# Performance work log

Measured on AMD Instinct MI355X. Metric: run time of the kernel, lower is better.

## Reference

```python
import jax, jax.numpy as jnp
import numpy as np

# init_kwargs constants
ALPHA = 0.1
BETA = 0.1
CAPACITY = 1000.0
IDX_LNN = 0   # feat_idx['ln(N+1)']
IDX_DOBS = 2  # feat_idx['D_observed']
IDX_RATE = 3  # feat_idx['pkt_rate']

N = 4_194_304
W = 4096  # number of windows (static upper bound on window ids)
EPS = 1e-6


def _masked_quantile75(vals, valid):
    """torch.quantile(vals[valid], 0.75) with linear interpolation, jit-safe."""
    s = jnp.sort(jnp.where(valid, vals, jnp.inf))
    n = jnp.sum(valid)
    pos = jnp.maximum(0.75 * (n - 1).astype(jnp.float32), 0.0)
    lo = jnp.floor(pos).astype(jnp.int32)
    hi = jnp.ceil(pos).astype(jnp.int32)
    frac = pos - lo.astype(jnp.float32)
    q = s[lo] * (1.0 - frac) + s[hi] * frac
    return jnp.where(n > 0, jnp.maximum(q, EPS), 1.0)


def setup_inputs() -> dict:
    key = jax.random.key(0)
    k1, k2, k3, k4, k5 = jax.random.split(key, 5)
    logits = jax.random.normal(k1, (N, 2), jnp.float32)
    y = jax.random.randint(k2, (N,), 0, 2)
    mask = jnp.ones((N,), bool)
    x_raw = jax.random.normal(k3, (N, 4), jnp.float32)
    window_idx = jax.random.randint(k4, (N,), 0, W)
    class_weights = jax.random.uniform(k5, (2,), jnp.float32, 0.5, 1.5)
    return {"logits": logits, "y": y, "mask": mask, "x_raw": x_raw,
            "window_idx": window_idx, "class_weights": class_weights}


def reference(logits, y, mask, x_raw, window_idx, class_weights):
    maskf = mask.astype(jnp.float32)
    any_mask = jnp.sum(maskf) > 0

    # L_data: weighted cross entropy over masked samples
    logp = jax.nn.log_softmax(logits, axis=1)
    nll = -jnp.take_along_axis(logp, y[:, None], axis=1)[:, 0]
    wy = class_weights[y]
    denom = jnp.sum(maskf * wy)
    l_data = jnp.sum(maskf * wy * nll) / jnp.maximum(denom, 1e-12)

    # per-window physics terms (vectorized segment reductions)
    valid = (window_idx >= 0) & mask
    vf = valid.astype(jnp.float32)
    attack_prob = jax.nn.softmax(logits, axis=1)[:, 1]
    flow_rate = jnp.maximum(x_raw[:, IDX_RATE], 0.0)
    d_obs = jnp.maximum(x_raw[:, IDX_DOBS], 0.0)
    # note: flow_vol (exp(lnN)-1) is computed in the original but never used in the loss

    ref_dobs = _masked_quantile75(d_obs, valid)

    seg = jnp.where(valid, window_idx, 0).astype(jnp.int32)
    pv = attack_prob * vf  # zeroed contributions for invalid rows
    cnt = jax.ops.segment_sum(vf, seg, num_segments=W)
    sum_p = jax.ops.segment_sum(pv, seg, num_segments=W)
    agg_rate = jax.ops.segment_sum(pv * flow_rate, seg, num_segments=W)
    sum_pd = jax.ops.segment_sum(pv * d_obs, seg, num_segments=W)

    include = ((cnt >= 2.0) & (sum_p >= EPS)).astype(jnp.float32)

    d_mean = sum_pd / (sum_p + EPS)
    rate_ratio = agg_rate / (CAPACITY + EPS)
    buildup = jax.nn.relu(rate_ratio - 1.0)
    flow_t = buildup * buildup
    rho = jnp.clip(rate_ratio, 0.0, 0.99)
    d_theory = 1.0 / (1.0 - rho + EPS)
    lat_t = jax.nn.relu(d_theory - d_mean / ref_dobs)

    n_inc = jnp.sum(include)
    safe_n = jnp.maximum(n_inc, 1.0)
    l_flow = jnp.where(n_inc > 0, jnp.sum(flow_t * include) / safe_n, 0.0)
    l_latency = jnp.where(n_inc > 0, jnp.sum(lat_t * include) / safe_n, 0.0)

    # empty-mask early return path
    l_data = jnp.where(any_mask, l_data, 0.0)
    l_flow = jnp.where(any_mask, l_flow, 0.0)
    l_latency = jnp.where(any_mask, l_latency, 0.0)
    l_total = l_data + ALPHA * l_flow + BETA * l_latency
    return (l_total, l_data, l_flow, l_latency)
```

## Files before the change

### kernel.cpp

```cpp
#include <hip/hip_runtime.h>

#define NWIN 4096
#define EPSF 1e-6f
#define GRID_MAIN 512
#define BLOCK_MAIN 512
#define NWAVES (BLOCK_MAIN / 64)

#define SCALE_P   2097152.0f
#define SCALE_R   131072.0f
#define INV_P     (1.0/2097152.0)
#define INV_R     (1.0/131072.0)

#define OFF_SEGU  256
#define OFF_H1    65792
#define OFF_H2    73984
#define OFF_H3    90368
#define OFF_CEP   98560
#define OFF_PART  131072

__device__ __forceinline__ unsigned make_key_raw(const float2* __restrict__ xzw,
                                                 const int* __restrict__ mask,
                                                 const int* __restrict__ widx, int i)
{
    int wi = widx[i];
    int m = mask[i];
    if (wi < 0 || !m) return 0x7F800000u;
    float d = fmaxf(xzw[2 * i + 1].x, 0.0f);
    unsigned k = __float_as_uint(d);
    return (k == 0x80000000u) ? 0u : k;
}

__device__ __forceinline__ void process_elem(
    float lgx, float lgy, int yi, int mi, float xz, float xw, int wi,
    float cw0, float cw1, unsigned* keyOut,
    float& num, float& den, unsigned& nv, unsigned& nm, unsigned& zc,
    unsigned* s_seg, unsigned* s_h1)
{
    float d = lgx - lgy;
    float ad = fabsf(d);
    float t = __expf(-ad);
    float inv1t = 1.0f / (1.0f + t);
    float l1p = __logf(1.0f + t);
    float s = yi ? d : -d;
    float nll = fmaxf(s, 0.0f) + l1p;
    float maskf = mi ? 1.0f : 0.0f;
    float wy = (yi ? cw1 : cw0) * maskf;
    nm += (mi != 0);
    num += wy * nll;
    den += wy;

    bool vq = (wi >= 0) && mi;
    float dob = fmaxf(xz, 0.0f);
    unsigned kraw = __float_as_uint(dob);
    kraw = (kraw == 0x80000000u) ? 0u : kraw;
    unsigned key = vq ? kraw : 0x7F800000u;
    *keyOut = key;
    nv += vq;
    zc += (key == 0u);

    atomicAdd(&s_h1[key >> 21], (key != 0u) ? 1u : 0u);

    bool sv = vq && ((unsigned)wi < NWIN);
    float sf = sv ? 1.0f : 0.0f;
    unsigned b = sv ? ((unsigned)wi << 2) : (4u * NWIN);
    float p = ((d > 0.0f) ? t : 1.0f) * inv1t;
    float rate = fmaxf(xw, 0.0f);
    atomicAdd(&s_seg[b],     sv ? 1u : 0u);
    atomicAdd(&s_seg[b | 1], (unsigned)(sf * p * SCALE_P + 0.5f));
    atomicAdd(&s_seg[b | 2], (unsigned)(sf * p * rate * SCALE_R + 0.5f));
    atomicAdd(&s_seg[b | 3], (unsigned)(sf * p * dob * SCALE_R + 0.5f));
}

extern "C" __global__ __launch_bounds__(BLOCK_MAIN)
void k_main(const float2* __restrict__ logits, const int* __restrict__ y,
            const int* __restrict__ mask, const float2* __restrict__ xzw,
            const int* __restrict__ widx, const float* __restrict__ cw,
            float* __restrict__ ce_part,
            unsigned* __restrict__ g_seg_u32, unsigned* __restrict__ part,
            unsigned* __restrict__ keys, unsigned* __restrict__ gh1,
            int use_part, int use_keys, int n)
{
    __shared__ unsigned s_seg[4 * NWIN + 4];
    __shared__ unsigned s_h1[2048];
    __shared__ float s_redf[2 * NWAVES];
    __shared__ unsigned s_redu[3 * NWAVES];
    for (int j = threadIdx.x; j < 4 * NWIN + 4; j += BLOCK_MAIN) s_seg[j] = 0u;
    for (int j = threadIdx.x; j < 2048; j += BLOCK_MAIN) s_h1[j] = 0u;
    __syncthreads();

    const float cw0 = cw[0], cw1 = cw[1];
    float num = 0.0f, den = 0.0f;
    unsigned nv = 0u, nm = 0u, zc = 0u;

    const int nth = GRID_MAIN * BLOCK_MAIN;
    const int gtid = blockIdx.x * BLOCK_MAIN + threadIdx.x;
    const int nq = n >> 2;

    const float4* lg4 = (const float4*)logits;
    const int4* y4p = (const int4*)y;
    const int4* m4p = (const int4*)mask;
    const int4* w4p = (const int4*)widx;

    for (int q = gtid; q < nq; q += nth) {
        float4 lgA = lg4[2 * q], lgB = lg4[2 * q + 1];
        int4 y4 = y4p[q], m4 = m4p[q], w4 = w4p[q];
        float2 z0 = xzw[8 * q + 1], z1 = xzw[8 * q + 3];
        float2 z2 = xzw[8 * q + 5], z3 = xzw[8 * q + 7];

        uint4 kq;
        process_elem(lgA.x, lgA.y, y4.x, m4.x, z0.x, z0.y, w4.x,
                     cw0, cw1, &kq.x, num, den, nv, nm, zc, s_seg, s_h1);
        process_elem(lgA.z, lgA.w, y4.y, m4.y, z1.x, z1.y, w4.y,
                     cw0, cw1, &kq.y, num, den, nv, nm, zc, s_seg, s_h1);
        process_elem(lgB.x, lgB.y, y4.z, m4.z, z2.x, z2.y, w4.z,
                     cw0, cw1, &kq.z, num, den, nv, nm, zc, s_seg, s_h1);
        process_elem(lgB.z, lgB.w, y4.w, m4.w, z3.x, z3.y, w4.w,
                     cw0, cw1, &kq.w, num, den, nv, nm, zc, s_seg, s_h1);
        if (use_keys) ((uint4*)keys)[q] = kq;
    }
    for (int i = (nq << 2) + gtid; i < n; i += nth) {
        float2 lg = logits[i];
        float2 zz = xzw[2 * i + 1];
        unsigned k;
        process_elem(lg.x, lg.y, y[i], mask[i], zz.x, zz.y, widx[i],
                     cw0, cw1, &k, num, den, nv, nm, zc, s_seg, s_h1);
        if (use_keys) keys[i] = k;
    }

    for (int off = 32; off > 0; off >>= 1) {
        num += __shfl_down(num, off);
        den += __shfl_down(den, off);
        nv  += __shfl_down(nv, off);
        nm  += __shfl_down(nm, off);
        zc  += __shfl_down(zc, off);
    }
    const int wid = threadIdx.x >> 6;
    if ((threadIdx.x & 63) == 0) {
        s_redf[wid] = num; s_redf[NWAVES + wid] = den;
        s_redu[wid] = nv; s_redu[NWAVES + wid] = nm; s_redu[2 * NWAVES + wid] = zc;
    }
    __syncthreads();
    if (threadIdx.x == 0) {
        float tn = 0.0f, td = 0.0f;
        unsigned ta = 0u, tb = 0u, tc = 0u;
        for (int w = 0; w < NWAVES; ++w) {
            tn += s_redf[w]; td += s_redf[NWAVES + w];
            ta += s_redu[w]; tb += s_redu[NWAVES + w]; tc += s_redu[2 * NWAVES + w];
        }
        float* cp = ce_part + blockIdx.x * 8;
        cp[0] = tn; cp[1] = td;
        ((unsigned*)cp)[2] = ta; ((unsigned*)cp)[3] = tb; ((unsigned*)cp)[4] = tc;
    }

    if (use_part) {
        uint4* dst = (uint4*)(part + (size_t)blockIdx.x * (4 * NWIN));
        const uint4* src = (const uint4*)s_seg;
        for (int j = threadIdx.x; j < NWIN; j += BLOCK_MAIN) dst[j] = src[j];
    } else {
        for (int j = threadIdx.x; j < 4 * NWIN; j += BLOCK_MAIN) {
            unsigned v = s_seg[j];
            if (v) atomicAdd(&g_seg_u32[j], v);
        }
    }
    for (int j = threadIdx.x; j < 2048; j += BLOCK_MAIN) {
        unsigned v = s_h1[j];
        if (v) atomicAdd(&gh1[j], v);
    }
}

__device__ void scan_search_g(const unsigned* __restrict__ gh, int NB, unsigned rank,
                              unsigned zadd, unsigned* sv, unsigned* wsb,
                              unsigned* ret)
{
    const int tid = threadIdx.x;
    const int B = blockDim.x;
    for (int j = tid; j < NB; j += B) sv[j] = gh[j] + ((j == 0) ? zadd : 0u);
    __syncthreads();
    const int E = NB / B;
    const int base = tid * E;
    unsigned loc = 0u;
    for (int e = 0; e < E; ++e) loc += sv[base + e];
    unsigned inc = loc;
    const int lane = tid & 63;
    for (int off = 1; off < 64; off <<= 1) {
        unsigned u = __shfl_up(inc, off);
        if (lane >= off) inc += u;
    }
    const int wid = tid >> 6;
    const int nw = B >> 6;
    if (lane == 63) wsb[wid] = inc;
    __syncthreads();
    if (tid == 0) {
        unsigned run = 0u;
        for (int w = 0; w < nw; ++w) { unsigned t = wsb[w]; wsb[w] = run; run += t; }
    }
    __syncthreads();
    unsigned c = wsb[wid] + (inc - loc);
    for (int e = 0; e < E; ++e) {
        unsigned hv = sv[base + e];
        if (rank >= c && rank < c + hv) { ret[0] = (unsigned)(base + e); ret[1] = rank - c; }
        c += hv;
    }
    __syncthreads();
}

extern "C" __global__ __launch_bounds__(512)
void k_post(const unsigned* __restrict__ part, unsigned* __restrict__ g_seg_u32,
            const float* __restrict__ ce_part, double* __restrict__ ws_d,
            unsigned* __restrict__ ws_u, float* __restrict__ ws_f,
            const unsigned* __restrict__ gh1, int use_part)
{
    if (blockIdx.x < 128) {
        if (!use_part) return;
        const int c = blockIdx.x >> 5;
        const int bin = (blockIdx.x & 31) * 512 + threadIdx.x;
        const unsigned* p = part + (size_t)c * 128 * (4 * NWIN) + bin;
        unsigned s = 0u;
#pragma unroll 8
        for (int b = 0; b < 128; ++b) s += p[(size_t)b * (4 * NWIN)];
        if (s) atomicAdd(&g_seg_u32[bin], s);
        return;
    }

    __shared__ unsigned sv[2048];
    __shared__ unsigned wsb[16];
    __shared__ unsigned ret[2];
    __shared__ double sd[2 * 8];
    __shared__ unsigned su[3 * 8];
    __shared__ unsigned bc[4];
    __shared__ float bf[1];

    const int tid = threadIdx.x;
    const float* cp = ce_part + tid * 8;
    double n_ = (double)cp[0];
    double d_ = (double)cp[1];
    unsigned a = ((const unsigned*)cp)[2];
    unsigned b = ((const unsigned*)cp)[3];
    unsigned c = ((const unsigned*)cp)[4];
    for (int off = 32; off > 0; off >>= 1) {
        n_ += __shfl_down(n_, off);
        d_ += __shfl_down(d_, off);
        a  += __shfl_down(a, off);
        b  += __shfl_down(b, off);
        c  += __shfl_down(c, off);
    }
    const int wid = tid >> 6;
    if ((tid & 63) == 0) { sd[wid] = n_; sd[8 + wid] = d_;
                           su[wid] = a; su[8 + wid] = b; su[16 + wid] = c; }
    __syncthreads();
    if (tid == 0) {
        double tn = 0.0, td = 0.0;
        unsigned ta = 0u, tb = 0u, tc = 0u;
        for (int w = 0; w < 8; ++w) {
            tn += sd[w]; td += sd[8 + w];
            ta += su[w]; tb += su[8 + w]; tc += su[16 + w];
        }
        ws_d[0] = tn; ws_d[1] = td;
        ws_u[4] = ta; ws_u[5] = tb;
        float nf = (float)((int)ta - 1);
        float pos = fmaxf(0.75f * nf, 0.0f);
        float lo = floorf(pos);
        bf[0] = pos - lo;
        bc[0] = tc;
        bc[1] = ta;
        bc[2] = (unsigned)lo;
        bc[3] = (unsigned)ceilf(pos);
    }
    __syncthreads();
    const unsigned zadd = bc[0];
    const unsigned r0 = bc[2], r1 = bc[3];
    if (tid == 0) ws_f[7] = bf[0];

    scan_search_g(gh1, 2048, r0, zadd, sv, wsb, ret);
    if (tid == 0) { ws_u[8] = ret[0]; ws_u[10] = ret[1]; }
    scan_search_g(gh1, 2048, r1, zadd, sv, wsb, ret);
    if (tid == 0) { ws_u[9] = ret[0]; ws_u[11] = ret[1]; }
}

__device__ __forceinline__ void h2_one(unsigned key, unsigned p0, unsigned p1,
                                       unsigned* h)
{
    unsigned top = key >> 21;
    unsigned sub = (key >> 10) & 2047u;
    if (top == p0) atomicAdd(&h[sub], 1u);
    if (top == p1) atomicAdd(&h[2048 + sub], 1u);
}

extern "C" __global__ __launch_bounds__(256)
void k_hist2(const unsigned* __restrict__ keys, const float2* __restrict__ xzw,
             const int* __restrict__ mask, const int* __restrict__ widx,
             int use_keys, int n, const unsigned* __restrict__ ws_u,
             unsigned* __restrict__ gh)
{
    __shared__ unsigned h[2 * 2048];
    for (int j = threadIdx.x; j < 2 * 2048; j += 256) h[j] = 0u;
    __syncthreads();
    const unsigned p0 = ws_u[8], p1 = ws_u[9];
    const int nthr = gridDim.x * blockDim.x;
    const int gtid = blockIdx.x * blockDim.x + threadIdx.x;
    const int nq = n >> 2;
    if (use_keys) {
        const uint4* k4 = (const uint4*)keys;
        int base = gtid;
        for (; base + 3 * nthr < nq; base += 4 * nthr) {
            uint4 a = k4[base], b = k4[base + nthr];
            uint4 c = k4[base + 2 * nthr], d = k4[base + 3 * nthr];
            h2_one(a.x, p0, p1, h); h2_one(a.y, p0, p1, h);
            h2_one(a.z, p0, p1, h); h2_one(a.w, p0, p1, h);
            h2_one(b.x, p0, p1, h); h2_one(b.y, p0, p1, h);
            h2_one(b.z, p0, p1, h); h2_one(b.w, p0, p1, h);
            h2_one(c.x, p0, p1, h); h2_one(c.y, p0, p1, h);
            h2_one(c.z, p0, p1, h); h2_one(c.w, p0, p1, h);
            h2_one(d.x, p0, p1, h); h2_one(d.y, p0, p1, h);
            h2_one(d.z, p0, p1, h); h2_one(d.w, p0, p1, h);
        }
        for (; base < nq; base += nthr) {
            uint4 a = k4[base];
            h2_one(a.x, p0, p1, h); h2_one(a.y, p0, p1, h);
            h2_one(a.z, p0, p1, h); h2_one(a.w, p0, p1, h);
        }
        for (int i = (nq << 2) + gtid; i < n; i += nthr)
            h2_one(keys[i], p0, p1, h);
    } else {
        for (int i = gtid; i < n; i += nthr)
            h2_one(make_key_raw(xzw, mask, widx, i), p0, p1, h);
    }
    __syncthreads();
    for (int j = threadIdx.x; j < 2 * 2048; j += 256)
        if (h[j]) atomicAdd(&gh[j], h[j]);
}

extern "C" __global__ __launch_bounds__(256)
void k_scan2(unsigned* __restrict__ ws_u, const unsigned* __restrict__ gh)
{
    __shared__ unsigned sv[2048];
    __shared__ unsigned wsb[16];
    __shared__ unsigned ret[2];
    unsigned p0 = ws_u[8], p1 = ws_u[9];
    unsigned r0 = ws_u[10], r1 = ws_u[11];
    scan_search_g(gh, 2048, r0, 0u, sv, wsb, ret);
    if (threadIdx.x == 0) { ws_u[8] = (p0 << 11) | ret[0]; ws_u[10] = ret[1]; }
    scan_search_g(gh + 2048, 2048, r1, 0u, sv, wsb, ret);
    if (threadIdx.x == 0) { ws_u[9] = (p1 << 11) | ret[0]; ws_u[11] = ret[1]; }
}

__device__ __forceinline__ void h3_one(unsigned key, unsigned p0, unsigned p1,
                                       unsigned* h)
{
    unsigned top = key >> 10;
    unsigned sub = key & 1023u;
    if (top == p0) atomicAdd(&h[sub], 1u);
    if (top == p1) atomicAdd(&h[1024 + sub], 1u);
}

extern "C" __global__ __launch_bounds__(256)
void k_hist3(const unsigned* __restrict__ keys, const float2* __restrict__ xzw,
             const int* __restrict__ mask, const int* __restrict__ widx,
             int use_keys, int n, const unsigned* __restrict__ ws_u,
             unsigned* __restrict__ gh)
{
    __shared__ unsigned h[2 * 1024];
    for (int j = threadIdx.x; j < 2 * 1024; j += 256) h[j] = 0u;
    __syncthreads();
    const unsigned p0 = ws_u[8], p1 = ws_u[9];
    const int nthr = gridDim.x * blockDim.x;
    const int gtid = blockIdx.x * blockDim.x + threadIdx.x;
    const int nq = n >> 2;
    if (use_keys) {
        const uint4* k4 = (const uint4*)keys;
        int base = gtid;
        for (; base + 3 * nthr < nq; base += 4 * nthr) {
            uint4 a = k4[base], b = k4[base + nthr];
            uint4 c = k4[base + 2 * nthr], d = k4[base + 3 * nthr];
            h3_one(a.x, p0, p1, h); h3_one(a.y, p0, p1, h);
            h3_one(a.z, p0, p1, h); h3_one(a.w, p0, p1, h);
            h3_one(b.x, p0, p1, h); h3_one(b.y, p0, p1, h);
            h3_one(b.z, p0, p1, h); h3_one(b.w, p0, p1, h);
            h3_one(c.x, p0, p1, h); h3_one(c.y, p0, p1, h);
            h3_one(c.z, p0, p1, h); h3_one(c.w, p0, p1, h);
            h3_one(d.x, p0, p1, h); h3_one(d.y, p0, p1, h);
            h3_one(d.z, p0, p1, h); h3_one(d.w, p0, p1, h);
        }
        for (; base < nq; base += nthr) {
            uint4 a = k4[base];
            h3_one(a.x, p0, p1, h); h3_one(a.y, p0, p1, h);
            h3_one(a.z, p0, p1, h); h3_one(a.w, p0, p1, h);
        }
        for (int i = (nq << 2) + gtid; i < n; i += nthr)
            h3_one(keys[i], p0, p1, h);
    } else {
        for (int i = gtid; i < n; i += nthr)
            h3_one(make_key_raw(xzw, mask, widx, i), p0, p1, h);
    }
    __syncthreads();
    for (int j = threadIdx.x; j < 2 * 1024; j += 256)
        if (h[j]) atomicAdd(&gh[j], h[j]);
}

extern "C" __global__ __launch_bounds__(1024)
void k_final(const unsigned* __restrict__ g_seg_u32, const double* __restrict__ ws_d,
             const float* __restrict__ ws_f, const unsigned* __restrict__ ws_u,
             const unsigned* __restrict__ gh3, float* __restrict__ out)
{
    __shared__ unsigned sv[1024];
    __shared__ unsigned wsb[16];
    __shared__ unsigned ret[2];
    __shared__ double red[48];

    const unsigned p0 = ws_u[8], p1 = ws_u[9];
    const unsigned r0 = ws_u[10], r1 = ws_u[11];
    scan_search_g(gh3, 1024, r0, 0u, sv, wsb, ret);
    const float v0 = __uint_as_float((p0 << 10) | ret[0]);
    scan_search_g(gh3 + 1024, 1024, r1, 0u, sv, wsb, ret);
    const float v1 = __uint_as_float((p1 << 10) | ret[0]);

    const int nvalid = (int)ws_u[4];
    const float frac = ws_f[7];
    const float qf = v0 * (1.0f - frac) + v1 * frac;
    const double ref = (double)((nvalid > 0) ? fmaxf(qf, EPSF) : 1.0f);

    const uint4* gs4 = (const uint4*)g_seg_u32;
    double ninc = 0.0, fsum = 0.0, lsum = 0.0;
    for (int w = threadIdx.x; w < NWIN; w += blockDim.x) {
        uint4 v = gs4[w];
        double c   = (double)v.x;
        double sp  = (double)v.y * INV_P;
        double ar  = (double)v.z * INV_R;
        double spd = (double)v.w * INV_R;
        double inc = (c >= 2.0 && sp >= 1e-6) ? 1.0 : 0.0;
        double dmean = spd / (sp + 1e-6);
        double rr = ar / (1000.0 + 1e-6);
        double bu = fmax(rr - 1.0, 0.0);
        double flow = bu * bu;
        double rho = fmin(fmax(rr, 0.0), 0.99);
        double dth = 1.0 / (1.0 - rho + 1e-6);
        double lat = fmax(dth - dmean / ref, 0.0);
        ninc += inc; fsum += flow * inc; lsum += lat * inc;
    }
    for (int off = 32; off > 0; off >>= 1) {
        ninc += __shfl_down(ninc, off);
        fsum += __shfl_down(fsum, off);
        lsum += __shfl_down(lsum, off);
    }
    int wid = threadIdx.x >> 6, lane = threadIdx.x & 63;
    if (lane == 0) { red[wid] = ninc; red[16 + wid] = fsum; red[32 + wid] = lsum; }
    __syncthreads();
    if (threadIdx.x == 0) {
        double n_i = 0.0, f_s = 0.0, l_s = 0.0;
        int nw = (int)blockDim.x >> 6;
        for (int w = 0; w < nw; ++w) { n_i += red[w]; f_s += red[16 + w]; l_s += red[32 + w]; }
        double safe = fmax(n_i, 1.0);
        double l_flow = (n_i > 0.0) ? f_s / safe : 0.0;
        double l_lat  = (n_i > 0.0) ? l_s / safe : 0.0;
        double den = ws_d[1];
        double l_data = ws_d[0] / fmax(den, 1e-12);
        bool any = ws_u[5] > 0u;
        if (!any) { l_data = 0.0; l_flow = 0.0; l_lat = 0.0; }
        out[0] = (float)(l_data + 0.1 * l_flow + 0.1 * l_lat);
        out[1] = (float)l_data;
        out[2] = (float)l_flow;
        out[3] = (float)l_lat;
    }
}

extern "C" void kernel_launch(void* const* d_in, const int* in_sizes, int n_in,
                              void* d_out, int out_size, void* d_ws, size_t ws_size,
                              hipStream_t stream)
{
    const float2* logits = (const float2*)d_in[0];
    const int* y = (const int*)d_in[1];
    const int* mask = (const int*)d_in[2];
    const float2* xzw = (const float2*)d_in[3];
    const int* widx = (const int*)d_in[4];
    const float* cw = (const float*)d_in[5];
    float* out = (float*)d_out;
    const int n = in_sizes[1];

    unsigned char* ws8 = (unsigned char*)d_ws;
    double* ws_d = (double*)ws8;
    float* ws_f = (float*)ws8;
    unsigned* ws_u = (unsigned*)ws8;
    unsigned* g_seg_u32 = (unsigned*)(ws8 + OFF_SEGU);
    unsigned* g_h1 = (unsigned*)(ws8 + OFF_H1);
    unsigned* g_h2 = (unsigned*)(ws8 + OFF_H2);
    unsigned* g_h3 = (unsigned*)(ws8 + OFF_H3);
    float* ce_part = (float*)(ws8 + OFF_CEP);

    const size_t part_bytes = (size_t)GRID_MAIN * 4 * NWIN * 4;
    const size_t keys_bytes = (size_t)n * 4u;
    size_t off = OFF_PART;
    int use_part = 0, use_keys = 0;
    unsigned* part = (unsigned*)(ws8 + off);
    if (ws_size >= off + part_bytes) { use_part = 1; off += part_bytes; }
    unsigned* keys = (unsigned*)(ws8 + off);
    if (ws_size >= off + keys_bytes) { use_keys = 1; }

    hipMemsetAsync(d_ws, 0, OFF_PART, stream);

    k_main<<<GRID_MAIN, BLOCK_MAIN, 0, stream>>>(logits, y, mask, xzw, widx, cw,
                                                 ce_part, g_seg_u32, part, keys,
                                                 g_h1, use_part, use_keys, n);
    k_post<<<129, 512, 0, stream>>>(part, g_seg_u32, ce_part, ws_d, ws_u, ws_f,
                                    g_h1, use_part);
    k_hist2<<<1024, 256, 0, stream>>>(keys, xzw, mask, widx, use_keys, n, ws_u, g_h2);
    k_scan2<<<1, 256, 0, stream>>>(ws_u, g_h2);
    k_hist3<<<1024, 256, 0, stream>>>(keys, xzw, mask, widx, use_keys, n, ws_u, g_h3);
    k_final<<<1, 1024, 0, stream>>>(g_seg_u32, ws_d, ws_f, ws_u, g_h3, out);
}
```

Before: 91.84 us.

## Pack segment count and histogram bins to shrink LDS and raise block count

Per-window shared accumulators shrink from four words to three by packing the count into the top 8 bits of the probability sum, whose scale is lowered so it fits in 24 bits. The first-level histogram now packs two 16-bit bins per word. The smaller LDS footprint is meant to fit more blocks per CU, and the grid grows to 768 blocks, with a fallback to 512 when workspace is short. The post-reduction unpacks the fields and loops over the variable grid. The risks are per-block overflow of the 8-bit count or 24-bit sum and lower precision in the probability sum.

```diff
diff --git a/kernel.cpp b/kernel.cpp
--- a/kernel.cpp
+++ b/kernel.cpp
@@ -2,13 +2,13 @@
 
 #define NWIN 4096
 #define EPSF 1e-6f
-#define GRID_MAIN 512
 #define BLOCK_MAIN 512
 #define NWAVES (BLOCK_MAIN / 64)
-
-#define SCALE_P   2097152.0f
+#define SEGW (3 * NWIN)
+
+#define SCALE_P   65536.0f
 #define SCALE_R   131072.0f
-#define INV_P     (1.0/2097152.0)
+#define INV_P     (1.0/65536.0)
 #define INV_R     (1.0/131072.0)
 
 #define OFF_SEGU  256
@@ -58,17 +58,19 @@
     nv += vq;
     zc += (key == 0u);
 
-    atomicAdd(&s_h1[key >> 21], (key != 0u) ? 1u : 0u);
+    unsigned hb = key >> 21;
+    atomicAdd(&s_h1[hb >> 1], (key != 0u) ? (1u << ((hb & 1u) << 4)) : 0u);
 
     bool sv = vq && ((unsigned)wi < NWIN);
-    float sf = sv ? 1.0f : 0.0f;
-    unsigned b = sv ? ((unsigned)wi << 2) : (4u * NWIN);
+    unsigned b = sv ? ((unsigned)wi * 3u) : 0u;
     float p = ((d > 0.0f) ? t : 1.0f) * inv1t;
     float rate = fmaxf(xw, 0.0f);
-    atomicAdd(&s_seg[b],     sv ? 1u : 0u);
-    atomicAdd(&s_seg[b | 1], (unsigned)(sf * p * SCALE_P + 0.5f));
-    atomicAdd(&s_seg[b | 2], (unsigned)(sf * p * rate * SCALE_R + 0.5f));
-    atomicAdd(&s_seg[b | 3], (unsigned)(sf * p * dob * SCALE_R + 0.5f));
+    unsigned a0 = sv ? ((1u << 24) | (unsigned)(p * SCALE_P + 0.5f)) : 0u;
+    unsigned a1 = sv ? (unsigned)(p * rate * SCALE_R + 0.5f) : 0u;
+    unsigned a2 = sv ? (unsigned)(p * dob * SCALE_R + 0.5f) : 0u;
+    atomicAdd(&s_seg[b], a0);
+    atomicAdd(&s_seg[b + 1], a1);
+    atomicAdd(&s_seg[b + 2], a2);
 }
 
 extern "C" __global__ __launch_bounds__(BLOCK_MAIN)
@@ -80,19 +82,19 @@
             unsigned* __restrict__ keys, unsigned* __restrict__ gh1,
             int use_part, int use_keys, int n)
 {
-    __shared__ unsigned s_seg[4 * NWIN + 4];
-    __shared__ unsigned s_h1[2048];
+    __shared__ unsigned s_seg[SEGW];
+    __shared__ unsigned s_h1[1024];
     __shared__ float s_redf[2 * NWAVES];
     __shared__ unsigned s_redu[3 * NWAVES];
-    for (int j = threadIdx.x; j < 4 * NWIN + 4; j += BLOCK_MAIN) s_seg[j] = 0u;
-    for (int j = threadIdx.x; j < 2048; j += BLOCK_MAIN) s_h1[j] = 0u;
+    for (int j = threadIdx.x; j < SEGW; j += BLOCK_MAIN) s_seg[j] = 0u;
+    for (int j = threadIdx.x; j < 1024; j += BLOCK_MAIN) s_h1[j] = 0u;
     __syncthreads();
 
     const float cw0 = cw[0], cw1 = cw[1];
     float num = 0.0f, den = 0.0f;
     unsigned nv = 0u, nm = 0u, zc = 0u;
 
-    const int nth = GRID_MAIN * BLOCK_MAIN;
+    const int nth = gridDim.x * BLOCK_MAIN;
     const int gtid = blockIdx.x * BLOCK_MAIN + threadIdx.x;
     const int nq = n >> 2;
 
@@ -153,18 +155,28 @@
     }
 
     if (use_part) {
-        uint4* dst = (uint4*)(part + (size_t)blockIdx.x * (4 * NWIN));
+        uint4* dst = (uint4*)(part + (size_t)blockIdx.x * SEGW);
         const uint4* src = (const uint4*)s_seg;
-        for (int j = threadIdx.x; j < NWIN; j += BLOCK_MAIN) dst[j] = src[j];
+        for (int j = threadIdx.x; j < SEGW / 4; j += BLOCK_MAIN) dst[j] = src[j];
     } else {
-        for (int j = threadIdx.x; j < 4 * NWIN; j += BLOCK_MAIN) {
+        for (int j = threadIdx.x; j < SEGW; j += BLOCK_MAIN) {
             unsigned v = s_seg[j];
-            if (v) atomicAdd(&g_seg_u32[j], v);
-        }
-    }
-    for (int j = threadIdx.x; j < 2048; j += BLOCK_MAIN) {
+            if (v) {
+                unsigned wi = (unsigned)j / 3u, t = (unsigned)j % 3u;
+                if (t == 0u) {
+                    atomicAdd(&g_seg_u32[(wi << 2)], v >> 24);
+                    atomicAdd(&g_seg_u32[(wi << 2) + 1], v & 0xFFFFFFu);
+                } else {
+                    atomicAdd(&g_seg_u32[(wi << 2) + 1 + t], v);
+                }
+            }
+        }
+    }
+    for (int j = threadIdx.x; j < 1024; j += BLOCK_MAIN) {
         unsigned v = s_h1[j];
-        if (v) atomicAdd(&gh1[j], v);
+        unsigned lo = v & 0xFFFFu, hi = v >> 16;
+        if (lo) atomicAdd(&gh1[2 * j], lo);
+        if (hi) atomicAdd(&gh1[2 * j + 1], hi);
     }
 }
 
@@ -208,17 +220,28 @@
 void k_post(const unsigned* __restrict__ part, unsigned* __restrict__ g_seg_u32,
             const float* __restrict__ ce_part, double* __restrict__ ws_d,
             unsigned* __restrict__ ws_u, float* __restrict__ ws_f,
-            const unsigned* __restrict__ gh1, int use_part)
-{
-    if (blockIdx.x < 128) {
+            const unsigned* __restrict__ gh1, int use_part, int grid)
+{
+    if (blockIdx.x < 96) {
         if (!use_part) return;
-        const int c = blockIdx.x >> 5;
-        const int bin = (blockIdx.x & 31) * 512 + threadIdx.x;
-        const unsigned* p = part + (size_t)c * 128 * (4 * NWIN) + bin;
-        unsigned s = 0u;
-#pragma unroll 8
-        for (int b = 0; b < 128; ++b) s += p[(size_t)b * (4 * NWIN)];
-        if (s) atomicAdd(&g_seg_u32[bin], s);
+        const int c = blockIdx.x / 24;
+        const int bin = (blockIdx.x % 24) * 512 + threadIdx.x;
+        const int per = grid >> 2;
+        const unsigned* p = part + (size_t)c * per * SEGW + bin;
+        const unsigned wi = (unsigned)bin / 3u, t = (unsigned)bin % 3u;
+        if (t == 0u) {
+            unsigned cnt = 0u, ps = 0u;
+            for (int b = 0; b < per; ++b) {
+                unsigned w = p[(size_t)b * SEGW];
+                cnt += w >> 24; ps += w & 0xFFFFFFu;
+            }
+            if (cnt) atomicAdd(&g_seg_u32[wi << 2], cnt);
+            if (ps)  atomicAdd(&g_seg_u32[(wi << 2) + 1], ps);
+        } else {
+            unsigned s = 0u;
+            for (int b = 0; b < per; ++b) s += p[(size_t)b * SEGW];
+            if (s) atomicAdd(&g_seg_u32[(wi << 2) + 1 + t], s);
+        }
         return;
     }
 
@@ -231,12 +254,16 @@
     __shared__ float bf[1];
 
     const int tid = threadIdx.x;
-    const float* cp = ce_part + tid * 8;
-    double n_ = (double)cp[0];
-    double d_ = (double)cp[1];
-    unsigned a = ((const unsigned*)cp)[2];
-    unsigned b = ((const unsigned*)cp)[3];
-    unsigned c = ((const unsigned*)cp)[4];
+    double n_ = 0.0, d_ = 0.0;
+    unsigned a = 0u, b = 0u, c = 0u;
+    for (int s0 = tid; s0 < grid; s0 += 512) {
+        const float* cp = ce_part + s0 * 8;
+        n_ += (double)cp[0];
+        d_ += (double)cp[1];
+        a += ((const unsigned*)cp)[2];
+        b += ((const unsigned*)cp)[3];
+        c += ((const unsigned*)cp)[4];
+    }
     for (int off = 32; off > 0; off >>= 1) {
         n_ += __shfl_down(n_, off);
         d_ += __shfl_down(d_, off);
@@ -262,7 +289,6 @@
         float lo = floorf(pos);
         bf[0] = pos - lo;
         bc[0] = tc;
-        bc[1] = ta;
         bc[2] = (unsigned)lo;
         bc[3] = (unsigned)ceilf(pos);
     }
@@ -486,22 +512,28 @@
     unsigned* g_h3 = (unsigned*)(ws8 + OFF_H3);
     float* ce_part = (float*)(ws8 + OFF_CEP);
 
-    const size_t part_bytes = (size_t)GRID_MAIN * 4 * NWIN * 4;
     const size_t keys_bytes = (size_t)n * 4u;
-    size_t off = OFF_PART;
+    int grid = 768;
     int use_part = 0, use_keys = 0;
-    unsigned* part = (unsigned*)(ws8 + off);
-    if (ws_size >= off + part_bytes) { use_part = 1; off += part_bytes; }
-    unsigned* keys = (unsigned*)(ws8 + off);
-    if (ws_size >= off + keys_bytes) { use_keys = 1; }
+    size_t part_bytes = 0;
+    for (;;) {
+        part_bytes = (size_t)grid * SEGW * 4u;
+        if (ws_size >= OFF_PART + part_bytes + keys_bytes) { use_part = 1; use_keys = 1; break; }
+        if (ws_size >= OFF_PART + part_bytes) { use_part = 1; break; }
+        if (grid == 768) { grid = 512; continue; }
+        if (ws_size >= OFF_PART + keys_bytes) use_keys = 1;
+        break;
+    }
+    unsigned* part = (unsigned*)(ws8 + OFF_PART);
+    unsigned* keys = (unsigned*)(ws8 + OFF_PART + (use_part ? part_bytes : 0));
 
     hipMemsetAsync(d_ws, 0, OFF_PART, stream);
 
-    k_main<<<GRID_MAIN, BLOCK_MAIN, 0, stream>>>(logits, y, mask, xzw, widx, cw,
-                                                 ce_part, g_seg_u32, part, keys,
-                                                 g_h1, use_part, use_keys, n);
-    k_post<<<129, 512, 0, stream>>>(part, g_seg_u32, ce_part, ws_d, ws_u, ws_f,
-                                    g_h1, use_part);
+    k_main<<<grid, BLOCK_MAIN, 0, stream>>>(logits, y, mask, xzw, widx, cw,
+                                            ce_part, g_seg_u32, part, keys,
+                                            g_h1, use_part, use_keys, n);
+    k_post<<<97, 512, 0, stream>>>(part, g_seg_u32, ce_part, ws_d, ws_u, ws_f,
+                                   g_h1, use_part, grid);
     k_hist2<<<1024, 256, 0, stream>>>(keys, xzw, mask, widx, use_keys, n, ws_u, g_h2);
     k_scan2<<<1, 256, 0, stream>>>(ws_u, g_h2);
     k_hist3<<<1024, 256, 0, stream>>>(keys, xzw, mask, widx, use_keys, n, ws_u, g_h3);
```

Result: slower. 149.0 us (+62.3%).
